# Kernel tuning notes

Measured on AMD Instinct MI355X. Metric: run time of the kernel, lower is better.

The kernel has to match this reference:

```python
import jax, jax.numpy as jnp
import numpy as np

LN_EPS = 1e-5

def _ln(x, g, b):
    m = jnp.mean(x, axis=-1, keepdims=True)
    v = jnp.mean(jnp.square(x - m), axis=-1, keepdims=True)
    return (x - m) / jnp.sqrt(v + LN_EPS) * g + b

def setup_inputs() -> dict:
    key = jax.random.key(0)
    ks = jax.random.split(key, 24)
    B, S, N = 8, 4096, 32
    H = 32          # self_dim // 2
    D = 64          # self_dim
    O = 32          # output_dim
    def w(k, shape):
        fan_in = shape[0]
        return jax.random.normal(k, shape, dtype=jnp.float32) / np.sqrt(fan_in)
    inp = {
        "expr": jax.random.normal(ks[0], (B, S), dtype=jnp.float32),
        "neighbors": jax.random.normal(ks[1], (B, N, S), dtype=jnp.float32),
        "edge_info": jax.random.normal(ks[2], (B, S, N), dtype=jnp.float32),
        "mask": jax.random.bernoulli(ks[3], 0.1, (B, S)),
        # neighbors branch: Linear(2,H), LN(H), ReLU, Linear(H,H)
        "nW1": w(ks[4], (2, H)), "nb1": jnp.zeros((H,), jnp.float32),
        "nlg": jnp.ones((H,), jnp.float32), "nlb": jnp.zeros((H,), jnp.float32),
        "nW2": w(ks[5], (H, H)), "nb2": jnp.zeros((H,), jnp.float32),
        # self branch: Linear(1,H), LN(H), ReLU, Linear(H,H)
        "sW1": w(ks[6], (1, H)), "sb1": jnp.zeros((H,), jnp.float32),
        "slg": jnp.ones((H,), jnp.float32), "slb": jnp.zeros((H,), jnp.float32),
        "sW2": w(ks[7], (H, H)), "sb2": jnp.zeros((H,), jnp.float32),
        # shared: Linear(D,D), LN(D), ReLU, Linear(D,O)
        "hW1": w(ks[8], (D, D)), "hb1": jnp.zeros((D,), jnp.float32),
        "hlg": jnp.ones((D,), jnp.float32), "hlb": jnp.zeros((D,), jnp.float32),
        "hW2": w(ks[9], (D, O)), "hb2": jnp.zeros((O,), jnp.float32),
    }
    return inp

def reference(expr, neighbors, edge_info, mask,
              nW1, nb1, nlg, nlb, nW2, nb2,
              sW1, sb1, slg, slb, sW2, sb2,
              hW1, hb1, hlg, hlb, hW2, hb2):
    # neighbors: (B,N,S) -> (B,S,N); pair with edge_info -> (B,S,N,2)
    nfeat = jnp.stack([jnp.transpose(neighbors, (0, 2, 1)), edge_info], axis=-1)
    h = nfeat @ nW1 + nb1                      # (B,S,N,H)
    h = jax.nn.relu(_ln(h, nlg, nlb))
    h = h @ nW2 + nb2
    nagg = jnp.sum(h, axis=-2)                 # (B,S,H)
    # self branch
    e = expr[..., None]                        # (B,S,1)
    e = e @ sW1 + sb1                          # (B,S,H)
    e = jax.nn.relu(_ln(e, slg, slb))
    e = e @ sW2 + sb2
    # shared
    x = jnp.concatenate([e, nagg], axis=-1)    # (B,S,2H)
    x = x @ hW1 + hb1
    x = jax.nn.relu(_ln(x, hlg, hlb))
    x = x @ hW2 + hb2                          # (B,S,O)
    x = jnp.where(mask[..., None], 0.0, x)
    return x
```

## Files before the change

kernel.cpp:

```cpp
#include <hip/hip_runtime.h>
#include <hip/hip_bf16.h>


#define LN_EPS 1e-5f

__global__ __launch_bounds__(256) void gnn_fold(
    const float* __restrict__ nW1, const float* __restrict__ nb1,
    const float* __restrict__ nlg, const float* __restrict__ nlb,
    const float* __restrict__ nW2, const float* __restrict__ nb2,
    const float* __restrict__ sW1, const float* __restrict__ sb1,
    const float* __restrict__ slg, const float* __restrict__ slb,
    const float* __restrict__ sW2, const float* __restrict__ sb2,
    const float* __restrict__ hW1, const float* __restrict__ hb1,
    float* __restrict__ ws)
{
    int tid = blockIdx.x * 256 + threadIdx.x;
    int k = tid >> 6, m = tid & 63;
    float acc = 0.f;
    if (k < 32) {
        #pragma unroll 8
        for (int i = 0; i < 32; ++i) acc = fmaf(sW2[k*32 + i], hW1[i*64 + m], acc);
    } else {
        int kk = k - 32;
        #pragma unroll 8
        for (int i = 0; i < 32; ++i) acc = fmaf(nW2[kk*32 + i], hW1[(32 + i)*64 + m], acc);
    }
    ws[256 + k*64 + m] = acc;

    if (blockIdx.x == 0) {
        int t = threadIdx.x;
        if (t < 64) {
            float c = hb1[t];
            for (int i = 0; i < 32; ++i) {
                c = fmaf(sb2[i], hW1[i*64 + t], c);
                c = fmaf(32.f * nb2[i], hW1[(32 + i)*64 + t], c);
            }
            ws[4352 + t] = c;
        } else if (t < 96) {
            int j = t - 64;
            float m0 = 0.f, m1 = 0.f, mb = 0.f;
            for (int i = 0; i < 32; ++i) { m0 += nW1[i]; m1 += nW1[32 + i]; mb += nb1[i]; }
            m0 *= (1.f/32.f); m1 *= (1.f/32.f); mb *= (1.f/32.f);
            float a = nW1[j] - m0, c = nW1[32 + j] - m1, d = nb1[j] - mb;
            ws[j]       = a * nlg[j];
            ws[32 + j]  = c * nlg[j];
            ws[64 + j]  = d * nlg[j];
            ws[96 + j]  = nlb[j];
            float ms = 0.f, msb = 0.f;
            for (int i = 0; i < 32; ++i) { ms += sW1[i]; msb += sb1[i]; }
            ms *= (1.f/32.f); msb *= (1.f/32.f);
            float as = sW1[j] - ms, ds = sb1[j] - msb;
            ws[134 + j] = as * slg[j];
            ws[166 + j] = ds * slg[j];
            ws[198 + j] = slb[j];
        } else if (t == 96) {
            float m0 = 0.f, m1 = 0.f, mb = 0.f;
            for (int i = 0; i < 32; ++i) { m0 += nW1[i]; m1 += nW1[32 + i]; mb += nb1[i]; }
            m0 *= (1.f/32.f); m1 *= (1.f/32.f); mb *= (1.f/32.f);
            float qaa=0,qcc=0,qdd=0,qac=0,qad=0,qcd=0;
            for (int j = 0; j < 32; ++j) {
                float a = nW1[j] - m0, c = nW1[32 + j] - m1, d = nb1[j] - mb;
                qaa += a*a; qcc += c*c; qdd += d*d; qac += a*c; qad += a*d; qcd += c*d;
            }
            ws[128]=qaa*(1.f/32.f); ws[129]=qcc*(1.f/32.f); ws[130]=qdd*(1.f/32.f);
            ws[131]=qac*(1.f/32.f); ws[132]=qad*(1.f/32.f); ws[133]=qcd*(1.f/32.f);
            float ms = 0.f, msb = 0.f;
            for (int i = 0; i < 32; ++i) { ms += sW1[i]; msb += sb1[i]; }
            ms *= (1.f/32.f); msb *= (1.f/32.f);
            float saa=0, sad=0, sdd=0;
            for (int j = 0; j < 32; ++j) {
                float as = sW1[j] - ms, ds = sb1[j] - msb;
                saa += as*as; sad += as*ds; sdd += ds*ds;
            }
            ws[230]=saa*(1.f/32.f); ws[231]=sad*(1.f/32.f); ws[232]=sdd*(1.f/32.f);
        }
    }
}

__global__ __launch_bounds__(256) void gnn_main(
    const float* __restrict__ expr, const float* __restrict__ neighbors,
    const float* __restrict__ edge_info, const int* __restrict__ mask,
    const float* __restrict__ hlg, const float* __restrict__ hlb,
    const float* __restrict__ hW2, const float* __restrict__ hb2,
    const float* __restrict__ ws, float* __restrict__ out)
{
    __shared__ float s_feat[64 * 33 * 2];
    __shared__ float s_inv[64 * 33];
    __shared__ float s_X[64 * 65];
    __shared__ float s_red[64 * 9];
    __shared__ float s_expr[64];

    const int t  = threadIdx.x;
    const int g0 = blockIdx.x * 64;
    const int bb = g0 >> 12;
    const int s0 = g0 & 4095;
    const float* nbp = neighbors + ((size_t)bb * 32 * 4096 + s0);
    const float* eip = edge_info + (size_t)g0 * 32;

    #pragma unroll
    for (int i = 0; i < 8; ++i) {
        int idx = i * 256 + t;
        int n = idx >> 6, col = idx & 63;
        s_feat[(col * 33 + n) * 2 + 0] = nbp[n * 4096 + col];
    }
    #pragma unroll
    for (int i = 0; i < 8; ++i) {
        int idx = i * 256 + t;
        int tok = idx >> 5, n = idx & 31;
        s_feat[(tok * 33 + n) * 2 + 1] = eip[idx];
    }
    if (t < 64) s_expr[t] = expr[g0 + t];
    __syncthreads();

    {
        float qaa = ws[128], qcc = ws[129], qdd = ws[130];
        float qac = ws[131], qad = ws[132], qcd = ws[133];
        #pragma unroll
        for (int i = 0; i < 8; ++i) {
            int idx = i * 256 + t;
            int tok = idx >> 5, n = idx & 31;
            float2 f = *(const float2*)&s_feat[(tok * 33 + n) * 2];
            float nb = f.x, ei = f.y;
            float v = qdd + nb * (qaa * nb + 2.f * qad) + ei * (qcc * ei + 2.f * qcd)
                    + 2.f * qac * nb * ei;
            s_inv[tok * 33 + n] = rsqrtf(v + LN_EPS);
        }
    }
    __syncthreads();

    const int tok = t >> 2;
    const int jb  = (t & 3) * 8;
    float Ag[8], Cg[8], Dg[8], lbv[8];
    #pragma unroll
    for (int i = 0; i < 8; ++i) {
        Ag[i]  = ws[jb + i];
        Cg[i]  = ws[32 + jb + i];
        Dg[i]  = ws[64 + jb + i];
        lbv[i] = ws[96 + jb + i];
    }
    float nsum[8] = {0,0,0,0,0,0,0,0};
    #pragma unroll 4
    for (int n = 0; n < 32; ++n) {
        float2 f  = *(const float2*)&s_feat[(tok * 33 + n) * 2];
        float inv = s_inv[tok * 33 + n];
        #pragma unroll
        for (int i = 0; i < 8; ++i) {
            float r = fmaf(f.x, Ag[i], Dg[i]);
            r = fmaf(f.y, Cg[i], r);
            r = fmaf(r, inv, lbv[i]);
            nsum[i] += fmaxf(r, 0.f);
        }
    }

    {
        float ex  = s_expr[tok];
        float saa = ws[230], sad = ws[231], sdd = ws[232];
        float vs  = fmaf(ex, fmaf(ex, saa, 2.f * sad), sdd);
        float invs = rsqrtf(vs + LN_EPS);
        #pragma unroll
        for (int i = 0; i < 8; ++i) {
            float r = fmaf(ex, ws[134 + jb + i], ws[166 + jb + i]);
            r = fmaf(r, invs, ws[198 + jb + i]);
            s_X[tok * 65 + jb + i]      = fmaxf(r, 0.f);
            s_X[tok * 65 + 32 + jb + i] = nsum[i];
        }
    }
    __syncthreads();

    const int w = __builtin_amdgcn_readfirstlane(t >> 6);
    const int l = t & 63;
    const float* Gp = ws + 256 + w * 16;
    const float* cv = ws + 4352 + w * 16;
    float y[16];
    #pragma unroll
    for (int i = 0; i < 16; ++i) y[i] = cv[i];
    #pragma unroll 4
    for (int k = 0; k < 64; ++k) {
        float xk = s_X[l * 65 + k];
        const float* gk = Gp + k * 64;
        #pragma unroll
        for (int i = 0; i < 16; ++i) y[i] = fmaf(xk, gk[i], y[i]);
    }

    float sm = 0.f, s2 = 0.f;
    #pragma unroll
    for (int i = 0; i < 16; ++i) { sm += y[i]; s2 = fmaf(y[i], y[i], s2); }
    s_red[l * 9 + w * 2 + 0] = sm;
    s_red[l * 9 + w * 2 + 1] = s2;
    __syncthreads();
    float tot = 0.f, tot2 = 0.f;
    #pragma unroll
    for (int r = 0; r < 4; ++r) {
        tot  += s_red[l * 9 + r * 2 + 0];
        tot2 += s_red[l * 9 + r * 2 + 1];
    }
    float mean = tot * (1.f / 64.f);
    float var  = tot2 * (1.f / 64.f) - mean * mean;
    float linv = rsqrtf(var + LN_EPS);
    #pragma unroll
    for (int i = 0; i < 16; ++i) {
        float v = (y[i] - mean) * linv;
        v = fmaf(v, hlg[w * 16 + i], hlb[w * 16 + i]);
        y[i] = fmaxf(v, 0.f);
    }
    #pragma unroll
    for (int i = 0; i < 16; ++i) s_X[l * 65 + w * 16 + i] = y[i];
    __syncthreads();

    const int ob = w * 8;
    float o[8];
    #pragma unroll
    for (int i = 0; i < 8; ++i) o[i] = hb2[ob + i];
    #pragma unroll 4
    for (int m = 0; m < 64; ++m) {
        float ym = s_X[l * 65 + m];
        const float* h2 = hW2 + m * 32 + ob;
        #pragma unroll
        for (int i = 0; i < 8; ++i) o[i] = fmaf(ym, h2[i], o[i]);
    }
    int mk = mask[g0 + l];
    float4 o0 = make_float4(o[0], o[1], o[2], o[3]);
    float4 o1 = make_float4(o[4], o[5], o[6], o[7]);
    if (mk) { o0 = make_float4(0.f,0.f,0.f,0.f); o1 = o0; }
    float4* op = (float4*)(out + (size_t)(g0 + l) * 32 + ob);
    op[0] = o0;
    op[1] = o1;
}

extern "C" void kernel_launch(void* const* d_in, const int* in_sizes, int n_in,
                              void* d_out, int out_size, void* d_ws, size_t ws_size,
                              hipStream_t stream) {
    const float* expr      = (const float*)d_in[0];
    const float* neighbors = (const float*)d_in[1];
    const float* edge_info = (const float*)d_in[2];
    const int*   mask      = (const int*)d_in[3];
    const float* nW1 = (const float*)d_in[4];
    const float* nb1 = (const float*)d_in[5];
    const float* nlg = (const float*)d_in[6];
    const float* nlb = (const float*)d_in[7];
    const float* nW2 = (const float*)d_in[8];
    const float* nb2 = (const float*)d_in[9];
    const float* sW1 = (const float*)d_in[10];
    const float* sb1 = (const float*)d_in[11];
    const float* slg = (const float*)d_in[12];
    const float* slb = (const float*)d_in[13];
    const float* sW2 = (const float*)d_in[14];
    const float* sb2 = (const float*)d_in[15];
    const float* hW1 = (const float*)d_in[16];
    const float* hb1 = (const float*)d_in[17];
    const float* hlg = (const float*)d_in[18];
    const float* hlb = (const float*)d_in[19];
    const float* hW2 = (const float*)d_in[20];
    const float* hb2 = (const float*)d_in[21];
    float* ws  = (float*)d_ws;
    float* out = (float*)d_out;

    gnn_fold<<<16, 256, 0, stream>>>(nW1, nb1, nlg, nlb, nW2, nb2,
                                     sW1, sb1, slg, slb, sW2, sb2,
                                     hW1, hb1, ws);
    gnn_main<<<512, 256, 0, stream>>>(expr, neighbors, edge_info, mask,
                                      hlg, hlb, hW2, hb2, ws, out);
}
```

Before: 122.0 us.

## Double threads per block, fuse LN variance into neighbor loop, vectorize loads

Moves gnn_main to 512 threads per block, with each thread handling half as many hidden or output columns in every stage. The s_inv pass and its barrier are removed: the per-neighbor inverse std is recomputed inline, which duplicates the rsqrt across the 8 threads sharing a token. Global loads of neighbors, edge_info and ws constants become float4, and the epsilon and factor-of-2 terms are pre-folded into the workspace constants. The intent is more parallelism and fewer global and LDS transactions per block, in exchange for redundant rsqrt work and more threads per block.

```diff
diff --git a/kernel.cpp b/kernel.cpp
--- a/kernel.cpp
+++ b/kernel.cpp
@@ -50,9 +50,9 @@
             for (int i = 0; i < 32; ++i) { ms += sW1[i]; msb += sb1[i]; }
             ms *= (1.f/32.f); msb *= (1.f/32.f);
             float as = sW1[j] - ms, ds = sb1[j] - msb;
-            ws[134 + j] = as * slg[j];
-            ws[166 + j] = ds * slg[j];
-            ws[198 + j] = slb[j];
+            ws[136 + j] = as * slg[j];
+            ws[168 + j] = ds * slg[j];
+            ws[200 + j] = slb[j];
         } else if (t == 96) {
             float m0 = 0.f, m1 = 0.f, mb = 0.f;
             for (int i = 0; i < 32; ++i) { m0 += nW1[i]; m1 += nW1[32 + i]; mb += nb1[i]; }
@@ -62,8 +62,12 @@
                 float a = nW1[j] - m0, c = nW1[32 + j] - m1, d = nb1[j] - mb;
                 qaa += a*a; qcc += c*c; qdd += d*d; qac += a*c; qad += a*d; qcd += c*d;
             }
-            ws[128]=qaa*(1.f/32.f); ws[129]=qcc*(1.f/32.f); ws[130]=qdd*(1.f/32.f);
-            ws[131]=qac*(1.f/32.f); ws[132]=qad*(1.f/32.f); ws[133]=qcd*(1.f/32.f);
+            ws[128] = qaa*(1.f/32.f);
+            ws[129] = qcc*(1.f/32.f);
+            ws[130] = qdd*(1.f/32.f) + LN_EPS;
+            ws[131] = 2.f*qac*(1.f/32.f);
+            ws[132] = 2.f*qad*(1.f/32.f);
+            ws[133] = 2.f*qcd*(1.f/32.f);
             float ms = 0.f, msb = 0.f;
             for (int i = 0; i < 32; ++i) { ms += sW1[i]; msb += sb1[i]; }
             ms *= (1.f/32.f); msb *= (1.f/32.f);
@@ -72,12 +76,14 @@
                 float as = sW1[j] - ms, ds = sb1[j] - msb;
                 saa += as*as; sad += as*ds; sdd += ds*ds;
             }
-            ws[230]=saa*(1.f/32.f); ws[231]=sad*(1.f/32.f); ws[232]=sdd*(1.f/32.f);
+            ws[232] = saa*(1.f/32.f);
+            ws[233] = 2.f*sad*(1.f/32.f);
+            ws[234] = sdd*(1.f/32.f) + LN_EPS;
         }
     }
 }
 
-__global__ __launch_bounds__(256) void gnn_main(
+__global__ __launch_bounds__(512, 4) void gnn_main(
     const float* __restrict__ expr, const float* __restrict__ neighbors,
     const float* __restrict__ edge_info, const int* __restrict__ mask,
     const float* __restrict__ hlg, const float* __restrict__ hlb,
@@ -85,9 +91,8 @@
     const float* __restrict__ ws, float* __restrict__ out)
 {
     __shared__ float s_feat[64 * 33 * 2];
-    __shared__ float s_inv[64 * 33];
     __shared__ float s_X[64 * 65];
-    __shared__ float s_red[64 * 9];
+    __shared__ float s_red[64 * 17];
     __shared__ float s_expr[64];
 
     const int t  = threadIdx.x;
@@ -97,54 +102,47 @@
     const float* nbp = neighbors + ((size_t)bb * 32 * 4096 + s0);
     const float* eip = edge_info + (size_t)g0 * 32;
 
-    #pragma unroll
-    for (int i = 0; i < 8; ++i) {
-        int idx = i * 256 + t;
-        int n = idx >> 6, col = idx & 63;
-        s_feat[(col * 33 + n) * 2 + 0] = nbp[n * 4096 + col];
-    }
-    #pragma unroll
-    for (int i = 0; i < 8; ++i) {
-        int idx = i * 256 + t;
-        int tok = idx >> 5, n = idx & 31;
-        s_feat[(tok * 33 + n) * 2 + 1] = eip[idx];
+    {
+        int n = t >> 4, c4 = t & 15;
+        float4 v = *(const float4*)&nbp[n * 4096 + c4 * 4];
+        int base = ((c4 * 4) * 33 + n) * 2;
+        s_feat[base      ] = v.x;
+        s_feat[base +  66] = v.y;
+        s_feat[base + 132] = v.z;
+        s_feat[base + 198] = v.w;
+    }
+    {
+        int tk = t >> 3, n4 = t & 7;
+        float4 v = *(const float4*)&eip[tk * 32 + n4 * 4];
+        int base = (tk * 33 + n4 * 4) * 2 + 1;
+        s_feat[base    ] = v.x;
+        s_feat[base + 2] = v.y;
+        s_feat[base + 4] = v.z;
+        s_feat[base + 6] = v.w;
     }
     if (t < 64) s_expr[t] = expr[g0 + t];
     __syncthreads();
 
-    {
-        float qaa = ws[128], qcc = ws[129], qdd = ws[130];
-        float qac = ws[131], qad = ws[132], qcd = ws[133];
-        #pragma unroll
-        for (int i = 0; i < 8; ++i) {
-            int idx = i * 256 + t;
-            int tok = idx >> 5, n = idx & 31;
-            float2 f = *(const float2*)&s_feat[(tok * 33 + n) * 2];
-            float nb = f.x, ei = f.y;
-            float v = qdd + nb * (qaa * nb + 2.f * qad) + ei * (qcc * ei + 2.f * qcd)
-                    + 2.f * qac * nb * ei;
-            s_inv[tok * 33 + n] = rsqrtf(v + LN_EPS);
-        }
-    }
-    __syncthreads();
-
-    const int tok = t >> 2;
-    const int jb  = (t & 3) * 8;
-    float Ag[8], Cg[8], Dg[8], lbv[8];
-    #pragma unroll
-    for (int i = 0; i < 8; ++i) {
-        Ag[i]  = ws[jb + i];
-        Cg[i]  = ws[32 + jb + i];
-        Dg[i]  = ws[64 + jb + i];
-        lbv[i] = ws[96 + jb + i];
-    }
-    float nsum[8] = {0,0,0,0,0,0,0,0};
-    #pragma unroll 4
+    const int tok = t >> 3;
+    const int jb  = (t & 7) * 4;
+    float Ag[4], Cg[4], Dg[4], lbv[4];
+    *(float4*)Ag  = *(const float4*)&ws[jb];
+    *(float4*)Cg  = *(const float4*)&ws[32 + jb];
+    *(float4*)Dg  = *(const float4*)&ws[64 + jb];
+    *(float4*)lbv = *(const float4*)&ws[96 + jb];
+    const float qaa  = ws[128], qcc  = ws[129], qddp = ws[130];
+    const float qac2 = ws[131], qad2 = ws[132], qcd2 = ws[133];
+
+    float nsum[4] = {0.f, 0.f, 0.f, 0.f};
+    #pragma unroll 8
     for (int n = 0; n < 32; ++n) {
-        float2 f  = *(const float2*)&s_feat[(tok * 33 + n) * 2];
-        float inv = s_inv[tok * 33 + n];
-        #pragma unroll
-        for (int i = 0; i < 8; ++i) {
+        float2 f = *(const float2*)&s_feat[(tok * 33 + n) * 2];
+        float v = fmaf(f.x, fmaf(qaa, f.x, qad2),
+                  fmaf(f.y, fmaf(qcc, f.y, qcd2),
+                  fmaf(qac2, f.x * f.y, qddp)));
+        float inv = rsqrtf(v);
+        #pragma unroll
+        for (int i = 0; i < 4; ++i) {
             float r = fmaf(f.x, Ag[i], Dg[i]);
             r = fmaf(f.y, Cg[i], r);
             r = fmaf(r, inv, lbv[i]);
@@ -153,14 +151,17 @@
     }
 
     {
-        float ex  = s_expr[tok];
-        float saa = ws[230], sad = ws[231], sdd = ws[232];
-        float vs  = fmaf(ex, fmaf(ex, saa, 2.f * sad), sdd);
-        float invs = rsqrtf(vs + LN_EPS);
-        #pragma unroll
-        for (int i = 0; i < 8; ++i) {
-            float r = fmaf(ex, ws[134 + jb + i], ws[166 + jb + i]);
-            r = fmaf(r, invs, ws[198 + jb + i]);
+        float ex = s_expr[tok];
+        float As[4], Ds[4], sl[4];
+        *(float4*)As = *(const float4*)&ws[136 + jb];
+        *(float4*)Ds = *(const float4*)&ws[168 + jb];
+        *(float4*)sl = *(const float4*)&ws[200 + jb];
+        float vs   = fmaf(ex, fmaf(ws[232], ex, ws[233]), ws[234]);
+        float invs = rsqrtf(vs);
+        #pragma unroll
+        for (int i = 0; i < 4; ++i) {
+            float r = fmaf(ex, As[i], Ds[i]);
+            r = fmaf(r, invs, sl[i]);
             s_X[tok * 65 + jb + i]      = fmaxf(r, 0.f);
             s_X[tok * 65 + 32 + jb + i] = nsum[i];
         }
@@ -169,62 +170,57 @@
 
     const int w = __builtin_amdgcn_readfirstlane(t >> 6);
     const int l = t & 63;
-    const float* Gp = ws + 256 + w * 16;
-    const float* cv = ws + 4352 + w * 16;
-    float y[16];
-    #pragma unroll
-    for (int i = 0; i < 16; ++i) y[i] = cv[i];
+    const float* Gp = ws + 256 + w * 8;
+    const float* cv = ws + 4352 + w * 8;
+    float y[8];
+    #pragma unroll
+    for (int i = 0; i < 8; ++i) y[i] = cv[i];
     #pragma unroll 4
     for (int k = 0; k < 64; ++k) {
         float xk = s_X[l * 65 + k];
         const float* gk = Gp + k * 64;
         #pragma unroll
-        for (int i = 0; i < 16; ++i) y[i] = fmaf(xk, gk[i], y[i]);
+        for (int i = 0; i < 8; ++i) y[i] = fmaf(xk, gk[i], y[i]);
     }
 
     float sm = 0.f, s2 = 0.f;
     #pragma unroll
-    for (int i = 0; i < 16; ++i) { sm += y[i]; s2 = fmaf(y[i], y[i], s2); }
-    s_red[l * 9 + w * 2 + 0] = sm;
-    s_red[l * 9 + w * 2 + 1] = s2;
+    for (int i = 0; i < 8; ++i) { sm += y[i]; s2 = fmaf(y[i], y[i], s2); }
+    s_red[l * 17 + w * 2 + 0] = sm;
+    s_red[l * 17 + w * 2 + 1] = s2;
     __syncthreads();
     float tot = 0.f, tot2 = 0.f;
     #pragma unroll
-    for (int r = 0; r < 4; ++r) {
-        tot  += s_red[l * 9 + r * 2 + 0];
-        tot2 += s_red[l * 9 + r * 2 + 1];
+    for (int r = 0; r < 8; ++r) {
+        tot  += s_red[l * 17 + r * 2 + 0];
+        tot2 += s_red[l * 17 + r * 2 + 1];
     }
     float mean = tot * (1.f / 64.f);
     float var  = tot2 * (1.f / 64.f) - mean * mean;
     float linv = rsqrtf(var + LN_EPS);
     #pragma unroll
-    for (int i = 0; i < 16; ++i) {
+    for (int i = 0; i < 8; ++i) {
         float v = (y[i] - mean) * linv;
-        v = fmaf(v, hlg[w * 16 + i], hlb[w * 16 + i]);
-        y[i] = fmaxf(v, 0.f);
-    }
-    #pragma unroll
-    for (int i = 0; i < 16; ++i) s_X[l * 65 + w * 16 + i] = y[i];
-    __syncthreads();
-
-    const int ob = w * 8;
-    float o[8];
-    #pragma unroll
-    for (int i = 0; i < 8; ++i) o[i] = hb2[ob + i];
+        v = fmaf(v, hlg[w * 8 + i], hlb[w * 8 + i]);
+        s_X[l * 65 + w * 8 + i] = fmaxf(v, 0.f);
+    }
+    __syncthreads();
+
+    const int ob = w * 4;
+    int mk = mask[g0 + l];
+    float o[4];
+    #pragma unroll
+    for (int i = 0; i < 4; ++i) o[i] = hb2[ob + i];
     #pragma unroll 4
     for (int m = 0; m < 64; ++m) {
         float ym = s_X[l * 65 + m];
         const float* h2 = hW2 + m * 32 + ob;
         #pragma unroll
-        for (int i = 0; i < 8; ++i) o[i] = fmaf(ym, h2[i], o[i]);
-    }
-    int mk = mask[g0 + l];
-    float4 o0 = make_float4(o[0], o[1], o[2], o[3]);
-    float4 o1 = make_float4(o[4], o[5], o[6], o[7]);
-    if (mk) { o0 = make_float4(0.f,0.f,0.f,0.f); o1 = o0; }
-    float4* op = (float4*)(out + (size_t)(g0 + l) * 32 + ob);
-    op[0] = o0;
-    op[1] = o1;
+        for (int i = 0; i < 4; ++i) o[i] = fmaf(ym, h2[i], o[i]);
+    }
+    float4 ov = make_float4(o[0], o[1], o[2], o[3]);
+    if (mk) ov = make_float4(0.f, 0.f, 0.f, 0.f);
+    *(float4*)(out + (size_t)(g0 + l) * 32 + ob) = ov;
 }
 
 extern "C" void kernel_launch(void* const* d_in, const int* in_sizes, int n_in,
@@ -258,6 +254,6 @@
     gnn_fold<<<16, 256, 0, stream>>>(nW1, nb1, nlg, nlb, nW2, nb2,
                                      sW1, sb1, slg, slb, sW2, sb2,
                                      hW1, hb1, ws);
-    gnn_main<<<512, 256, 0, stream>>>(expr, neighbors, edge_info, mask,
+    gnn_main<<<512, 512, 0, stream>>>(expr, neighbors, edge_info, mask,
                                       hlg, hlb, hW2, hb2, ws, out);
 }
```

New measurement: 121.7 us. No clear change (-0.3%).
